# Optimization experiments

Hardware: AMD Instinct MI355X
Metric: run time of the kernel (lower is better)

Reference implementation:

```python
import jax, jax.numpy as jnp
import numpy as np

N_NODES = 100000
N_EDGES = 3200000
N_GRAPHS = 64
EPS = 1e-5

def setup_inputs() -> dict:
    key = jax.random.key(0)
    ks = jax.random.split(key, 12)
    x = jax.random.normal(ks[0], (N_NODES, 3), dtype=jnp.float32)
    edge_index = jax.random.randint(ks[1], (2, N_EDGES), 0, N_NODES, dtype=jnp.int64)
    edge_attr = jax.random.uniform(ks[2], (N_EDGES, 2), dtype=jnp.float32)
    batch = jnp.sort(jax.random.randint(ks[3], (N_NODES,), 0, N_GRAPHS, dtype=jnp.int64))
    # SplineConv kernels: [kernel_size^dim = 4, in, out]
    W1 = jax.random.normal(ks[4], (4, 3, 16), dtype=jnp.float32) * 0.3
    g1 = jnp.ones((16,), jnp.float32); b1 = jnp.zeros((16,), jnp.float32)
    W2 = jax.random.normal(ks[5], (4, 16, 32), dtype=jnp.float32) * 0.15
    g2 = jnp.ones((32,), jnp.float32); b2 = jnp.zeros((32,), jnp.float32)
    fc_w = jax.random.normal(ks[6], (10, 32), dtype=jnp.float32) * 0.15
    return {"x": x, "edge_index": edge_index, "edge_attr": edge_attr, "batch": batch,
            "W1": W1, "g1": g1, "b1": b1, "W2": W2, "g2": g2, "b2": b2, "fc_w": fc_w}

def _spline_basis(edge_attr):
    # degree=1, kernel_size=2, open spline: v = p*(K-degree)=p in [0,1), floor(v)=0
    # per-dim weights (1-p, p); flattened kernel index k = i0 + 2*i1
    p0, p1 = edge_attr[:, 0], edge_attr[:, 1]
    w0 = jnp.stack([1.0 - p0, p0], axis=-1)  # [E,2] over i0
    w1 = jnp.stack([1.0 - p1, p1], axis=-1)  # [E,2] over i1
    return (w1[:, :, None] * w0[:, None, :]).reshape(-1, 4)  # [E,4], k=i0+2*i1

def _spline_conv(x, src, dst, basis, W, n_nodes):
    # message per edge: sum_k basis[e,k] * (x[src[e]] @ W[k]); mean-aggregate at dst
    msg = jnp.einsum('ek,kio,ei->eo', basis, W, x[src])
    agg = jax.ops.segment_sum(msg, dst, num_segments=n_nodes)
    cnt = jax.ops.segment_sum(jnp.ones((src.shape[0],), x.dtype), dst, num_segments=n_nodes)
    return agg / jnp.maximum(cnt, 1.0)[:, None]

def _batchnorm(x, gamma, beta):
    mu = jnp.mean(x, axis=0)
    var = jnp.mean((x - mu) ** 2, axis=0)  # biased, as torch uses for normalization
    return (x - mu) * jax.lax.rsqrt(var + EPS) * gamma + beta

def reference(x, edge_index, edge_attr, batch, W1, g1, b1, W2, g2, b2, fc_w):
    src, dst = edge_index[0], edge_index[1]
    basis = _spline_basis(edge_attr)  # [E,4]
    h = jax.nn.elu(_spline_conv(x, src, dst, basis, W1, N_NODES))
    h = _batchnorm(h, g1, b1)
    h = jax.nn.elu(_spline_conv(h, src, dst, basis, W2, N_NODES))
    h = _batchnorm(h, g2, b2)
    # global mean pool over graphs
    s = jax.ops.segment_sum(h, batch, num_segments=N_GRAPHS)
    c = jax.ops.segment_sum(jnp.ones((h.shape[0],), h.dtype), batch, num_segments=N_GRAPHS)
    gm = s / jnp.maximum(c, 1.0)[:, None]
    return gm @ fc_w.T  # [N_GRAPHS, 10]
```

## Files before the change

kernel.cpp:

```cpp
#include <hip/hip_runtime.h>
#include <hip/hip_fp16.h>
#include <math.h>

#define NN 100000
#define NE 3200000
#define NG 64
#define EPSF 1e-5f
#define NB 391
#define BSH 8

#define OFF_ST1     0
#define OFF_ST2     32
#define OFF_GPOOL   96
#define OFF_BCNT    2144
#define ZERO_FLOATS 2536
#define OFF_BBASE   2536
#define OFF_BCUR    2928
#define OFF_OFFS    3320
#define OFF_STARTS  103324
#define OFF_H1      103392
#define OFF_H2      903392
#define OFF_RECSA   4103392
#define OFF_RECSB   10503392

__device__ __forceinline__ void atomAdd(float* p, float v) {
#if defined(__gfx90a__) || defined(__gfx940__) || defined(__gfx941__) || defined(__gfx942__) || defined(__gfx950__)
    unsafeAtomicAdd(p, v);
#else
    atomicAdd(p, v);
#endif
}

__device__ __forceinline__ float eluf(float x) { return x > 0.f ? x : expm1f(x); }

#define INV32767 (1.f / 32767.f)

__global__ void starts_k(const int* __restrict__ batch, int* __restrict__ starts) {
    int g = threadIdx.x;
    if (g > NG) return;
    int lo = 0, hi = NN;
    while (lo < hi) { int mid = (lo + hi) >> 1; if (batch[mid] < g) lo = mid + 1; else hi = mid; }
    starts[g] = lo;
}

__global__ void __launch_bounds__(256) bcount_k(const int* __restrict__ ei,
                                                int* __restrict__ bcnt) {
    __shared__ int lh[NB];
    int tid = threadIdx.x;
    for (int i = tid; i < NB; i += 256) lh[i] = 0;
    __syncthreads();
    const int4* d4 = (const int4*)(ei + NE);
    int base4 = blockIdx.x * 2048;
#pragma unroll
    for (int j = 0; j < 8; ++j) {
        int idx = base4 + j * 256 + tid;
        if (idx < NE / 4) {
            int4 d = d4[idx];
            atomicAdd(&lh[d.x >> BSH], 1);
            atomicAdd(&lh[d.y >> BSH], 1);
            atomicAdd(&lh[d.z >> BSH], 1);
            atomicAdd(&lh[d.w >> BSH], 1);
        }
    }
    __syncthreads();
    for (int i = tid; i < NB; i += 256)
        if (lh[i] > 0) atomicAdd(&bcnt[i], lh[i]);
}

__global__ void bscan_k(const int* __restrict__ bcnt, int* __restrict__ bbase,
                        int* __restrict__ bcur, int* __restrict__ offs) {
    __shared__ int s[512];
    int tid = threadIdx.x;
    int v = (tid < NB) ? bcnt[tid] : 0;
    s[tid] = v;
    __syncthreads();
    for (int d = 1; d < 512; d <<= 1) {
        int t = (tid >= (unsigned)d) ? s[tid - d] : 0;
        __syncthreads();
        s[tid] += t;
        __syncthreads();
    }
    if (tid < NB) {
        int e = s[tid] - v;
        bbase[tid] = e;
        bcur[tid] = e;
    }
    if (tid == 0) { bbase[NB] = NE; offs[NN] = NE; }
}

__global__ void __launch_bounds__(256) passA(const int* __restrict__ ei,
        const float* __restrict__ ea, int* __restrict__ bcur,
        uint2* __restrict__ recsA) {
    __shared__ int lh[NB];
    __shared__ int gcur[NB];
    int tid = threadIdx.x;
    for (int i = tid; i < NB; i += 256) lh[i] = 0;
    __syncthreads();
    int base = blockIdx.x * 4096;
    uint2 rec[16];
    int bk[16];
#pragma unroll
    for (int j = 0; j < 16; ++j) {
        int e = base + j * 256 + tid;
        bk[j] = -1;
        if (e < NE) {
            int src = ei[e];
            int dst = ei[NE + e];
            float2 p = ((const float2*)ea)[e];
            unsigned q0 = (unsigned)__float2uint_rn(p.x * 32767.f);
            unsigned q1 = (unsigned)__float2uint_rn(p.y * 32767.f);
            rec[j] = make_uint2((unsigned)src | (q0 << 17), (unsigned)dst | (q1 << 17));
            bk[j] = dst >> BSH;
            atomicAdd(&lh[bk[j]], 1);
        }
    }
    __syncthreads();
    for (int i = tid; i < NB; i += 256)
        if (lh[i] > 0) gcur[i] = atomicAdd(&bcur[i], lh[i]);
    __syncthreads();
#pragma unroll
    for (int j = 0; j < 16; ++j) {
        if (bk[j] >= 0) {
            int pos = atomicAdd(&gcur[bk[j]], 1);
            recsA[pos] = rec[j];
        }
    }
}

__global__ void __launch_bounds__(256) fine_k(const int* __restrict__ bbase,
        const uint2* __restrict__ recsA, int* __restrict__ offs,
        uint2* __restrict__ recsB) {
    __shared__ int cnt[256];
    __shared__ int sc[256];
    __shared__ int cur[256];
    int b = blockIdx.x;
    int tid = threadIdx.x;
    int rbeg = bbase[b], rend = bbase[b + 1];
    cnt[tid] = 0;
    __syncthreads();
    for (int i = rbeg + tid; i < rend; i += 256) {
        int d = (int)(recsA[i].y & 0x1FFFFu) & 255;
        atomicAdd(&cnt[d], 1);
    }
    __syncthreads();
    int v = cnt[tid];
    sc[tid] = v;
    __syncthreads();
    for (int d = 1; d < 256; d <<= 1) {
        int t = (tid >= (unsigned)d) ? sc[tid - d] : 0;
        __syncthreads();
        sc[tid] += t;
        __syncthreads();
    }
    int excl = sc[tid] - v;
    cur[tid] = excl;
    int node = (b << BSH) + tid;
    if (node < NN) offs[node] = rbeg + excl;
    __syncthreads();
    for (int i = rbeg + tid; i < rend; i += 256) {
        uint2 rc = recsA[i];
        int d = (int)(rc.y & 0x1FFFFu) & 255;
        int rank = atomicAdd(&cur[d], 1);
        recsB[rbeg + rank] = rc;
    }
}

__global__ void __launch_bounds__(256) conv1_gather(const int* __restrict__ offs,
        const uint2* __restrict__ recs, const float* __restrict__ x,
        const float* __restrict__ W1, __half* __restrict__ h1) {
    __shared__ float sW[192];
    if (threadIdx.x < 192) sW[threadIdx.x] = W1[threadIdx.x];
    __syncthreads();
    int t = blockIdx.x * blockDim.x + threadIdx.x;
    int n = t >> 2, sub = t & 3;
    if (n >= NN) return;
    int off = offs[n], end = offs[n + 1];
    float T[12];
#pragma unroll
    for (int i = 0; i < 12; ++i) T[i] = 0.f;
    for (int e = off + sub; e < end; e += 4) {
        uint2 r = recs[e];
        int s = (int)(r.x & 0x1FFFFu);
        float p0 = (float)(r.x >> 17) * INV32767;
        float p1 = (float)(r.y >> 17) * INV32767;
        float b0 = (1.f - p1) * (1.f - p0), b1 = (1.f - p1) * p0;
        float b2 = p1 * (1.f - p0), b3 = p1 * p0;
        float x0 = x[3 * s], x1 = x[3 * s + 1], x2 = x[3 * s + 2];
        T[0] = fmaf(b0, x0, T[0]);  T[1] = fmaf(b0, x1, T[1]);  T[2]  = fmaf(b0, x2, T[2]);
        T[3] = fmaf(b1, x0, T[3]);  T[4] = fmaf(b1, x1, T[4]);  T[5]  = fmaf(b1, x2, T[5]);
        T[6] = fmaf(b2, x0, T[6]);  T[7] = fmaf(b2, x1, T[7]);  T[8]  = fmaf(b2, x2, T[8]);
        T[9] = fmaf(b3, x0, T[9]);  T[10]= fmaf(b3, x1, T[10]); T[11] = fmaf(b3, x2, T[11]);
    }
    float ov[16];
#pragma unroll
    for (int o = 0; o < 16; ++o) {
        float acc = 0.f;
#pragma unroll
        for (int k = 0; k < 4; ++k)
#pragma unroll
            for (int i = 0; i < 3; ++i)
                acc = fmaf(T[k * 3 + i], sW[k * 48 + i * 16 + o], acc);
        acc += __shfl_xor(acc, 1);
        acc += __shfl_xor(acc, 2);
        ov[o] = acc;
    }
    if (sub != 0) return;
    float inv = 1.f / fmaxf((float)(end - off), 1.f);
    __half2 hh[8];
#pragma unroll
    for (int q = 0; q < 8; ++q)
        hh[q] = __float22half2_rn(make_float2(eluf(ov[2 * q] * inv),
                                              eluf(ov[2 * q + 1] * inv)));
    uint4* hp = (uint4*)(h1 + (long)n * 16);
    hp[0] = *(uint4*)&hh[0];
    hp[1] = *(uint4*)&hh[4];
}

__global__ void bn_sum16h(const __half2* __restrict__ h, float* __restrict__ st) {
    __shared__ float ss[16], sq[16];
    if (threadIdx.x < 16) { ss[threadIdx.x] = 0.f; sq[threadIdx.x] = 0.f; }
    __syncthreads();
    const int total = NN * 8;
    const int stride = gridDim.x * blockDim.x;
    float a0 = 0.f, a1 = 0.f, q0 = 0.f, q1 = 0.f;
    for (int i = blockIdx.x * blockDim.x + threadIdx.x; i < total; i += stride) {
        float2 f = __half22float2(h[i]);
        a0 += f.x; q0 += f.x * f.x;
        a1 += f.y; q1 += f.y * f.y;
    }
#pragma unroll
    for (int d = 8; d < 64; d <<= 1) {
        a0 += __shfl_xor(a0, d); q0 += __shfl_xor(q0, d);
        a1 += __shfl_xor(a1, d); q1 += __shfl_xor(q1, d);
    }
    int lane = threadIdx.x & 63;
    if (lane < 8) {
        atomicAdd(&ss[2 * lane], a0);     atomicAdd(&sq[2 * lane], q0);
        atomicAdd(&ss[2 * lane + 1], a1); atomicAdd(&sq[2 * lane + 1], q1);
    }
    __syncthreads();
    if (threadIdx.x < 16) {
        atomAdd(&st[threadIdx.x], ss[threadIdx.x]);
        atomAdd(&st[16 + threadIdx.x], sq[threadIdx.x]);
    }
}

__global__ void bn_sum32(const float* __restrict__ h, float* __restrict__ st) {
    __shared__ float ss[32], sq[32];
    if (threadIdx.x < 32) { ss[threadIdx.x] = 0.f; sq[threadIdx.x] = 0.f; }
    __syncthreads();
    const int total = NN * 32;
    const int stride = gridDim.x * blockDim.x;
    float a = 0.f, q = 0.f;
    for (int i = blockIdx.x * blockDim.x + threadIdx.x; i < total; i += stride) {
        float v = h[i];
        a += v; q += v * v;
    }
    a += __shfl_xor(a, 32);
    q += __shfl_xor(q, 32);
    int lane = threadIdx.x & 63;
    if (lane < 32) { atomicAdd(&ss[lane], a); atomicAdd(&sq[lane], q); }
    __syncthreads();
    if (threadIdx.x < 32) {
        atomAdd(&st[threadIdx.x], ss[threadIdx.x]);
        atomAdd(&st[32 + threadIdx.x], sq[threadIdx.x]);
    }
}

__global__ void __launch_bounds__(256) conv2_gather(const int* __restrict__ offs,
        const uint2* __restrict__ recs, const __half* __restrict__ h1,
        const float* __restrict__ st1, const float* __restrict__ g1,
        const float* __restrict__ b1v, const float* __restrict__ W2,
        float* __restrict__ h2) {
    __shared__ float s_sc[16], s_sh[16];
    __shared__ float sWp[2048];
    __shared__ float sV[128];
    if (threadIdx.x < 16) {
        int c = threadIdx.x;
        float mu = st1[c] * (1.f / NN);
        float var = st1[16 + c] * (1.f / NN) - mu * mu;
        float rs = rsqrtf(var + EPSF);
        float s = g1[c] * rs;
        s_sc[c] = s;
        s_sh[c] = b1v[c] - mu * s;
    }
    __syncthreads();
    for (int idx = threadIdx.x; idx < 2048; idx += blockDim.x) {
        int i = (idx & 511) >> 5;
        sWp[idx] = s_sc[i] * W2[idx];
    }
    if (threadIdx.x < 128) {
        int k = threadIdx.x >> 5, o = threadIdx.x & 31;
        float acc = 0.f;
#pragma unroll
        for (int i = 0; i < 16; ++i) acc = fmaf(s_sh[i], W2[k * 512 + i * 32 + o], acc);
        sV[threadIdx.x] = acc;
    }
    __syncthreads();
    int t = blockIdx.x * blockDim.x + threadIdx.x;
    int n = t >> 2, sub = t & 3;
    if (n >= NN) return;
    int off = offs[n], end = offs[n + 1];
    float U[64];
    float S0 = 0.f, S1 = 0.f, S2 = 0.f, S3 = 0.f;
#pragma unroll
    for (int i = 0; i < 64; ++i) U[i] = 0.f;
    for (int e = off + sub; e < end; e += 4) {
        uint2 r = recs[e];
        int s = (int)(r.x & 0x1FFFFu);
        float p0 = (float)(r.x >> 17) * INV32767;
        float p1 = (float)(r.y >> 17) * INV32767;
        float b0 = (1.f - p1) * (1.f - p0), b1 = (1.f - p1) * p0;
        float b2 = p1 * (1.f - p0), b3 = p1 * p0;
        const uint4* hp = (const uint4*)(h1 + (long)s * 16);
        uint4 ua = hp[0], ub = hp[1];
        float2 f0 = __half22float2(*(const __half2*)&ua.x);
        float2 f1 = __half22float2(*(const __half2*)&ua.y);
        float2 f2 = __half22float2(*(const __half2*)&ua.z);
        float2 f3 = __half22float2(*(const __half2*)&ua.w);
        float2 f4 = __half22float2(*(const __half2*)&ub.x);
        float2 f5 = __half22float2(*(const __half2*)&ub.y);
        float2 f6 = __half22float2(*(const __half2*)&ub.z);
        float2 f7 = __half22float2(*(const __half2*)&ub.w);
        float hv[16] = {f0.x, f0.y, f1.x, f1.y, f2.x, f2.y, f3.x, f3.y,
                        f4.x, f4.y, f5.x, f5.y, f6.x, f6.y, f7.x, f7.y};
#pragma unroll
        for (int i = 0; i < 16; ++i) {
            U[i]      = fmaf(b0, hv[i], U[i]);
            U[16 + i] = fmaf(b1, hv[i], U[16 + i]);
            U[32 + i] = fmaf(b2, hv[i], U[32 + i]);
            U[48 + i] = fmaf(b3, hv[i], U[48 + i]);
        }
        S0 += b0; S1 += b1; S2 += b2; S3 += b3;
    }
    float4 acc[8];
#pragma unroll
    for (int ob = 0; ob < 8; ++ob) acc[ob] = make_float4(0.f, 0.f, 0.f, 0.f);
    const float4* Wp4 = (const float4*)sWp;
#pragma unroll 4
    for (int ki = 0; ki < 64; ++ki) {
        float u = U[ki];
#pragma unroll
        for (int ob = 0; ob < 8; ++ob) {
            float4 w = Wp4[ki * 8 + ob];
            acc[ob].x = fmaf(u, w.x, acc[ob].x);
            acc[ob].y = fmaf(u, w.y, acc[ob].y);
            acc[ob].z = fmaf(u, w.z, acc[ob].z);
            acc[ob].w = fmaf(u, w.w, acc[ob].w);
        }
    }
    const float4* V4 = (const float4*)sV;
    float Sarr[4] = {S0, S1, S2, S3};
#pragma unroll
    for (int k = 0; k < 4; ++k) {
        float u = Sarr[k];
#pragma unroll
        for (int ob = 0; ob < 8; ++ob) {
            float4 w = V4[k * 8 + ob];
            acc[ob].x = fmaf(u, w.x, acc[ob].x);
            acc[ob].y = fmaf(u, w.y, acc[ob].y);
            acc[ob].z = fmaf(u, w.z, acc[ob].z);
            acc[ob].w = fmaf(u, w.w, acc[ob].w);
        }
    }
#pragma unroll
    for (int ob = 0; ob < 8; ++ob) {
        acc[ob].x += __shfl_xor(acc[ob].x, 1); acc[ob].x += __shfl_xor(acc[ob].x, 2);
        acc[ob].y += __shfl_xor(acc[ob].y, 1); acc[ob].y += __shfl_xor(acc[ob].y, 2);
        acc[ob].z += __shfl_xor(acc[ob].z, 1); acc[ob].z += __shfl_xor(acc[ob].z, 2);
        acc[ob].w += __shfl_xor(acc[ob].w, 1); acc[ob].w += __shfl_xor(acc[ob].w, 2);
    }
    if (sub != 0) return;
    float inv = 1.f / fmaxf((float)(end - off), 1.f);
    float4* out4 = (float4*)(h2 + (long)n * 32);
#pragma unroll
    for (int ob = 0; ob < 8; ++ob) {
        float4 a = acc[ob];
        a.x = eluf(a.x * inv); a.y = eluf(a.y * inv);
        a.z = eluf(a.z * inv); a.w = eluf(a.w * inv);
        out4[ob] = a;
    }
}

__global__ void pool_k(const float* __restrict__ h2pre, const float* __restrict__ st2,
                       const float* __restrict__ g2, const float* __restrict__ b2v,
                       const int* __restrict__ batch, float* __restrict__ gpool) {
    int t = blockIdx.x * blockDim.x + threadIdx.x;
    int c = t & 31;
    int chunk = t >> 5;
    if (chunk >= NN / 32) return;
    float mu = st2[c] * (1.f / NN);
    float var = st2[32 + c] * (1.f / NN) - mu * mu;
    float rs = rsqrtf(var + EPSF);
    float s = g2[c] * rs;
    float sh = b2v[c] - mu * s;
    int n0 = chunk * 32;
    int g_cur = batch[n0];
    float acc = 0.f;
    for (int i = 0; i < 32; ++i) {
        int n = n0 + i;
        int g = batch[n];
        float v = fmaf(h2pre[(long)n * 32 + c], s, sh);
        if (g != g_cur) {
            atomAdd(gpool + g_cur * 32 + c, acc);
            acc = 0.f;
            g_cur = g;
        }
        acc += v;
    }
    atomAdd(gpool + g_cur * 32 + c, acc);
}

__global__ void final_k(const float* __restrict__ gpool, const int* __restrict__ starts,
                        const float* __restrict__ fc, float* __restrict__ out) {
    int t = blockIdx.x * blockDim.x + threadIdx.x;
    if (t >= NG * 10) return;
    int g = t / 10, j = t - g * 10;
    float cg = (float)(starts[g + 1] - starts[g]);
    float inv = 1.f / fmaxf(cg, 1.f);
    float sv = 0.f;
#pragma unroll
    for (int ch = 0; ch < 32; ++ch) sv = fmaf(gpool[g * 32 + ch], fc[j * 32 + ch], sv);
    out[t] = sv * inv;
}

extern "C" void kernel_launch(void* const* d_in, const int* in_sizes, int n_in,
                              void* d_out, int out_size, void* d_ws, size_t ws_size,
                              hipStream_t stream) {
    const float* x     = (const float*)d_in[0];
    const int*   ei    = (const int*)d_in[1];
    const float* ea    = (const float*)d_in[2];
    const int*   batch = (const int*)d_in[3];
    const float* W1    = (const float*)d_in[4];
    const float* g1    = (const float*)d_in[5];
    const float* b1v   = (const float*)d_in[6];
    const float* W2    = (const float*)d_in[7];
    const float* g2    = (const float*)d_in[8];
    const float* b2v   = (const float*)d_in[9];
    const float* fc    = (const float*)d_in[10];
    float* ws = (float*)d_ws;

    float*  st1    = ws + OFF_ST1;
    float*  st2    = ws + OFF_ST2;
    float*  gpool  = ws + OFF_GPOOL;
    int*    bcnt   = (int*)(ws + OFF_BCNT);
    int*    bbase  = (int*)(ws + OFF_BBASE);
    int*    bcur   = (int*)(ws + OFF_BCUR);
    int*    offs   = (int*)(ws + OFF_OFFS);
    int*    starts = (int*)(ws + OFF_STARTS);
    __half* h1     = (__half*)(ws + OFF_H1);
    float*  h2     = ws + OFF_H2;
    uint2*  recsA  = (uint2*)(ws + OFF_RECSA);
    uint2*  recsB  = (uint2*)(ws + OFF_RECSB);

    hipMemsetAsync(ws, 0, (size_t)ZERO_FLOATS * sizeof(float), stream);
    starts_k<<<1, 128, 0, stream>>>(batch, starts);

    const int BLK = 256;
    const int NGRID4 = (NN * 4 + BLK - 1) / BLK;

    bcount_k<<<391, BLK, 0, stream>>>(ei, bcnt);
    bscan_k<<<1, 512, 0, stream>>>(bcnt, bbase, bcur, offs);
    passA<<<(NE + 4095) / 4096, BLK, 0, stream>>>(ei, ea, bcur, recsA);
    fine_k<<<NB, BLK, 0, stream>>>(bbase, recsA, offs, recsB);
    conv1_gather<<<NGRID4, BLK, 0, stream>>>(offs, recsB, x, W1, h1);
    bn_sum16h<<<512, BLK, 0, stream>>>((const __half2*)h1, st1);
    conv2_gather<<<NGRID4, BLK, 0, stream>>>(offs, recsB, h1, st1, g1, b1v, W2, h2);
    bn_sum32<<<512, BLK, 0, stream>>>(h2, st2);
    pool_k<<<(NN + BLK - 1) / BLK, BLK, 0, stream>>>(h2, st2, g2, b2v, batch, gpool);
    final_k<<<3, BLK, 0, stream>>>(gpool, starts, fc, (float*)d_out);
}
```

Baseline: 376.0 us.

## Split conv2 gather across 8 lanes per node, one kernel slice each

conv2_gather now assigns 8 threads per node: each thread owns one of the 4 spline kernel slices and half of the edges. Each thread keeps 16 accumulators instead of 64 and does a 16x32 projection instead of 64x32, which cuts register pressure and should raise occupancy. In exchange, every h1 row is loaded by 4 threads instead of 1, and the reduction needs an extra shuffle stage.

```diff
diff --git a/kernel.cpp b/kernel.cpp
--- a/kernel.cpp
+++ b/kernel.cpp
@@ -298,77 +298,70 @@
     }
     __syncthreads();
     int t = blockIdx.x * blockDim.x + threadIdx.x;
-    int n = t >> 2, sub = t & 3;
+    int n = t >> 3, sub = t & 7;
     if (n >= NN) return;
+    int k = sub & 3, half = sub >> 2;
     int off = offs[n], end = offs[n + 1];
-    float U[64];
-    float S0 = 0.f, S1 = 0.f, S2 = 0.f, S3 = 0.f;
-#pragma unroll
-    for (int i = 0; i < 64; ++i) U[i] = 0.f;
-    for (int e = off + sub; e < end; e += 4) {
+    float Uk[16];
+#pragma unroll
+    for (int i = 0; i < 16; ++i) Uk[i] = 0.f;
+    float Sk = 0.f;
+    for (int e = off + half; e < end; e += 2) {
         uint2 r = recs[e];
         int s = (int)(r.x & 0x1FFFFu);
         float p0 = (float)(r.x >> 17) * INV32767;
         float p1 = (float)(r.y >> 17) * INV32767;
-        float b0 = (1.f - p1) * (1.f - p0), b1 = (1.f - p1) * p0;
-        float b2 = p1 * (1.f - p0), b3 = p1 * p0;
+        float f0 = (k & 1) ? p0 : 1.f - p0;
+        float f1 = (k & 2) ? p1 : 1.f - p1;
+        float bk = f0 * f1;
         const uint4* hp = (const uint4*)(h1 + (long)s * 16);
         uint4 ua = hp[0], ub = hp[1];
-        float2 f0 = __half22float2(*(const __half2*)&ua.x);
-        float2 f1 = __half22float2(*(const __half2*)&ua.y);
-        float2 f2 = __half22float2(*(const __half2*)&ua.z);
-        float2 f3 = __half22float2(*(const __half2*)&ua.w);
-        float2 f4 = __half22float2(*(const __half2*)&ub.x);
-        float2 f5 = __half22float2(*(const __half2*)&ub.y);
-        float2 f6 = __half22float2(*(const __half2*)&ub.z);
-        float2 f7 = __half22float2(*(const __half2*)&ub.w);
-        float hv[16] = {f0.x, f0.y, f1.x, f1.y, f2.x, f2.y, f3.x, f3.y,
-                        f4.x, f4.y, f5.x, f5.y, f6.x, f6.y, f7.x, f7.y};
-#pragma unroll
-        for (int i = 0; i < 16; ++i) {
-            U[i]      = fmaf(b0, hv[i], U[i]);
-            U[16 + i] = fmaf(b1, hv[i], U[16 + i]);
-            U[32 + i] = fmaf(b2, hv[i], U[32 + i]);
-            U[48 + i] = fmaf(b3, hv[i], U[48 + i]);
-        }
-        S0 += b0; S1 += b1; S2 += b2; S3 += b3;
+        float2 f0v = __half22float2(*(const __half2*)&ua.x);
+        float2 f1v = __half22float2(*(const __half2*)&ua.y);
+        float2 f2v = __half22float2(*(const __half2*)&ua.z);
+        float2 f3v = __half22float2(*(const __half2*)&ua.w);
+        float2 f4v = __half22float2(*(const __half2*)&ub.x);
+        float2 f5v = __half22float2(*(const __half2*)&ub.y);
+        float2 f6v = __half22float2(*(const __half2*)&ub.z);
+        float2 f7v = __half22float2(*(const __half2*)&ub.w);
+        Uk[0]  = fmaf(bk, f0v.x, Uk[0]);  Uk[1]  = fmaf(bk, f0v.y, Uk[1]);
+        Uk[2]  = fmaf(bk, f1v.x, Uk[2]);  Uk[3]  = fmaf(bk, f1v.y, Uk[3]);
+        Uk[4]  = fmaf(bk, f2v.x, Uk[4]);  Uk[5]  = fmaf(bk, f2v.y, Uk[5]);
+        Uk[6]  = fmaf(bk, f3v.x, Uk[6]);  Uk[7]  = fmaf(bk, f3v.y, Uk[7]);
+        Uk[8]  = fmaf(bk, f4v.x, Uk[8]);  Uk[9]  = fmaf(bk, f4v.y, Uk[9]);
+        Uk[10] = fmaf(bk, f5v.x, Uk[10]); Uk[11] = fmaf(bk, f5v.y, Uk[11]);
+        Uk[12] = fmaf(bk, f6v.x, Uk[12]); Uk[13] = fmaf(bk, f6v.y, Uk[13]);
+        Uk[14] = fmaf(bk, f7v.x, Uk[14]); Uk[15] = fmaf(bk, f7v.y, Uk[15]);
+        Sk += bk;
     }
     float4 acc[8];
-#pragma unroll
-    for (int ob = 0; ob < 8; ++ob) acc[ob] = make_float4(0.f, 0.f, 0.f, 0.f);
-    const float4* Wp4 = (const float4*)sWp;
-#pragma unroll 4
-    for (int ki = 0; ki < 64; ++ki) {
-        float u = U[ki];
+    const float4* V4 = (const float4*)(sV + k * 32);
+#pragma unroll
+    for (int ob = 0; ob < 8; ++ob) {
+        float4 v = V4[ob];
+        acc[ob] = make_float4(Sk * v.x, Sk * v.y, Sk * v.z, Sk * v.w);
+    }
+    const float4* Wk4 = (const float4*)(sWp + k * 512);
+#pragma unroll
+    for (int i = 0; i < 16; ++i) {
+        float u = Uk[i];
 #pragma unroll
         for (int ob = 0; ob < 8; ++ob) {
-            float4 w = Wp4[ki * 8 + ob];
+            float4 w = Wk4[i * 8 + ob];
             acc[ob].x = fmaf(u, w.x, acc[ob].x);
             acc[ob].y = fmaf(u, w.y, acc[ob].y);
             acc[ob].z = fmaf(u, w.z, acc[ob].z);
             acc[ob].w = fmaf(u, w.w, acc[ob].w);
         }
     }
-    const float4* V4 = (const float4*)sV;
-    float Sarr[4] = {S0, S1, S2, S3};
-#pragma unroll
-    for (int k = 0; k < 4; ++k) {
-        float u = Sarr[k];
-#pragma unroll
-        for (int ob = 0; ob < 8; ++ob) {
-            float4 w = V4[k * 8 + ob];
-            acc[ob].x = fmaf(u, w.x, acc[ob].x);
-            acc[ob].y = fmaf(u, w.y, acc[ob].y);
-            acc[ob].z = fmaf(u, w.z, acc[ob].z);
-            acc[ob].w = fmaf(u, w.w, acc[ob].w);
-        }
-    }
 #pragma unroll
     for (int ob = 0; ob < 8; ++ob) {
-        acc[ob].x += __shfl_xor(acc[ob].x, 1); acc[ob].x += __shfl_xor(acc[ob].x, 2);
-        acc[ob].y += __shfl_xor(acc[ob].y, 1); acc[ob].y += __shfl_xor(acc[ob].y, 2);
-        acc[ob].z += __shfl_xor(acc[ob].z, 1); acc[ob].z += __shfl_xor(acc[ob].z, 2);
-        acc[ob].w += __shfl_xor(acc[ob].w, 1); acc[ob].w += __shfl_xor(acc[ob].w, 2);
+        acc[ob].x += __shfl_xor(acc[ob].x, 1); acc[ob].y += __shfl_xor(acc[ob].y, 1);
+        acc[ob].z += __shfl_xor(acc[ob].z, 1); acc[ob].w += __shfl_xor(acc[ob].w, 1);
+        acc[ob].x += __shfl_xor(acc[ob].x, 2); acc[ob].y += __shfl_xor(acc[ob].y, 2);
+        acc[ob].z += __shfl_xor(acc[ob].z, 2); acc[ob].w += __shfl_xor(acc[ob].w, 2);
+        acc[ob].x += __shfl_xor(acc[ob].x, 4); acc[ob].y += __shfl_xor(acc[ob].y, 4);
+        acc[ob].z += __shfl_xor(acc[ob].z, 4); acc[ob].w += __shfl_xor(acc[ob].w, 4);
     }
     if (sub != 0) return;
     float inv = 1.f / fmaxf((float)(end - off), 1.f);
@@ -457,15 +450,14 @@
     starts_k<<<1, 128, 0, stream>>>(batch, starts);
 
     const int BLK = 256;
-    const int NGRID4 = (NN * 4 + BLK - 1) / BLK;
 
     bcount_k<<<391, BLK, 0, stream>>>(ei, bcnt);
     bscan_k<<<1, 512, 0, stream>>>(bcnt, bbase, bcur, offs);
     passA<<<(NE + 4095) / 4096, BLK, 0, stream>>>(ei, ea, bcur, recsA);
     fine_k<<<NB, BLK, 0, stream>>>(bbase, recsA, offs, recsB);
-    conv1_gather<<<NGRID4, BLK, 0, stream>>>(offs, recsB, x, W1, h1);
+    conv1_gather<<<(NN * 4 + BLK - 1) / BLK, BLK, 0, stream>>>(offs, recsB, x, W1, h1);
     bn_sum16h<<<512, BLK, 0, stream>>>((const __half2*)h1, st1);
-    conv2_gather<<<NGRID4, BLK, 0, stream>>>(offs, recsB, h1, st1, g1, b1v, W2, h2);
+    conv2_gather<<<(NN * 8 + BLK - 1) / BLK, BLK, 0, stream>>>(offs, recsB, h1, st1, g1, b1v, W2, h2);
     bn_sum32<<<512, BLK, 0, stream>>>(h2, st2);
     pool_k<<<(NN + BLK - 1) / BLK, BLK, 0, stream>>>(h2, st2, g2, b2v, batch, gpool);
     final_k<<<3, BLK, 0, stream>>>(gpool, starts, fc, (float*)d_out);
```

Result: faster. 354.6 us (-5.7%).
